# Performance work log

Measured on AMD Instinct MI355X. Metric: run time of the kernel, lower is better.

## Reference

```python
import jax, jax.numpy as jnp
import numpy as np

B, S, D, H, L, F = 1, 2048, 768, 12, 2, 3072
DH = D // H          # 64
W = 256              # one-sided sliding window (attention_window=512 total)
NC = S // W          # number of query chunks
VOCAB = 50265


def _ln(x, s, b, eps=1e-5):
    m = x.mean(-1, keepdims=True)
    v = ((x - m) ** 2).mean(-1, keepdims=True)
    return (x - m) / jnp.sqrt(v + eps) * s + b


def setup_inputs() -> dict:
    key = jax.random.key(0)
    ks = jax.random.split(key, 16)
    p = lambda k, sh: jax.random.normal(k, sh, jnp.float32) * 0.02
    return {
        "input_ids": jax.random.randint(ks[0], (B, S), 0, VOCAB),
        "attention_mask": jnp.ones((B, S), jnp.int32),
        "word_emb": p(ks[1], (VOCAB, D)),
        "pos_emb": p(ks[2], (S + 2, D)),          # roberta-style pos ids start at 2
        "type_emb": p(ks[3], (1, D)),
        "emb_ln_s": jnp.ones((D,), jnp.float32),
        "emb_ln_b": jnp.zeros((D,), jnp.float32),
        "Wqkv": p(ks[4], (L, 3, D, D)),
        "bqkv": jnp.zeros((L, 3, D), jnp.float32),
        "Wo": p(ks[5], (L, D, D)),
        "bo": jnp.zeros((L, D), jnp.float32),
        "ln1_s": jnp.ones((L, D), jnp.float32),
        "ln1_b": jnp.zeros((L, D), jnp.float32),
        "W1": p(ks[6], (L, D, F)),
        "b1": jnp.zeros((L, F), jnp.float32),
        "W2": p(ks[7], (L, F, D)),
        "b2": jnp.zeros((L, D), jnp.float32),
        "ln2_s": jnp.ones((L, D), jnp.float32),
        "ln2_b": jnp.zeros((L, D), jnp.float32),
        "pool_W": p(ks[8], (D, D)),
        "pool_b": jnp.zeros((D,), jnp.float32),
    }


def reference(input_ids, attention_mask, word_emb, pos_emb, type_emb,
              emb_ln_s, emb_ln_b, Wqkv, bqkv, Wo, bo, ln1_s, ln1_b,
              W1, b1, W2, b2, ln2_s, ln2_b, pool_W, pool_b):
    # ---- embeddings (roberta/longformer style) ----
    pos_ids = jnp.cumsum(attention_mask, axis=1) * attention_mask + 1  # padding_idx=1
    x = word_emb[input_ids] + pos_emb[pos_ids] + type_emb[0]
    x = _ln(x, emb_ln_s, emb_ln_b)

    # ---- banded-attention index/mask precompute (int constants) ----
    idx = jnp.arange(NC)[:, None] * W + jnp.arange(3 * W)[None, :]      # [NC, 3W] into padded seq
    rel = (jnp.arange(3 * W)[None, :] - W) - jnp.arange(W)[:, None]     # key_pos - query_pos
    band = (rel >= -W) & (rel <= W)                                      # [W, 3W]
    kmask = jnp.pad(attention_mask, ((0, 0), (W, W)))[:, idx].astype(bool)  # [B, NC, 3W]
    valid = band[None, None] & kmask[:, :, None, :]                      # [B, NC, W, 3W]

    inv_sqrt_dh = 1.0 / np.sqrt(DH)
    for l in range(L):
        qkv = jnp.einsum('bsd,tde->tbse', x, Wqkv[l]) + bqkv[l][:, None, None, :]
        q, k, v = [t.reshape(B, S, H, DH).transpose(0, 2, 1, 3) for t in qkv]  # [B,H,S,DH]
        qc = q.reshape(B, H, NC, W, DH)
        kp = jnp.pad(k, ((0, 0), (0, 0), (W, W), (0, 0)))
        vp = jnp.pad(v, ((0, 0), (0, 0), (W, W), (0, 0)))
        kc = kp[:, :, idx]                                               # [B,H,NC,3W,DH]
        vc = vp[:, :, idx]
        scores = jnp.einsum('bhcqd,bhckd->bhcqk', qc, kc) * inv_sqrt_dh  # [B,H,NC,W,3W]
        scores = jnp.where(valid[:, None], scores, -1e9)
        attn = jax.nn.softmax(scores, axis=-1)
        ctx = jnp.einsum('bhcqk,bhckd->bhcqd', attn, vc)
        ctx = ctx.reshape(B, H, S, DH).transpose(0, 2, 1, 3).reshape(B, S, D)
        x = _ln(x + ctx @ Wo[l] + bo[l], ln1_s[l], ln1_b[l])
        h = jax.nn.gelu(x @ W1[l] + b1[l], approximate=False)
        x = _ln(x + h @ W2[l] + b2[l], ln2_s[l], ln2_b[l])

    pooled = jnp.tanh(x[:, 0] @ pool_W + pool_b)
    return x, pooled
```

## Files before the change

### kernel.cpp

```cpp
#include <hip/hip_runtime.h>
#include <hip/hip_bf16.h>
#include <math.h>
#include <stddef.h>
#include <stdint.h>

typedef __hip_bfloat16 bf16;
typedef short bf16x8 __attribute__((ext_vector_type(8)));
typedef float f32x4 __attribute__((ext_vector_type(4)));

#define CS 2048
#define CD 768
#define CH 12
#define CDH 64
#define CF 3072
#define CW 256
#define CL 2
#define QKVN 2304
#define SDC ((size_t)CS * CD)
#define EPS_LD 136

__device__ __forceinline__ void gload_lds16(const bf16* g, bf16* l) {
  __builtin_amdgcn_global_load_lds(
      (const __attribute__((address_space(1))) void*)g,
      (__attribute__((address_space(3))) void*)l, 16, 0, 0);
}

__device__ __forceinline__ unsigned short f2bu(float v) {
  bf16 b = __float2bfloat16(v);
  return *(unsigned short*)&b;
}
__device__ __forceinline__ float bu2f(unsigned short u) {
  bf16 b = *(bf16*)&u;
  return __bfloat162float(b);
}

template<int NW>
__device__ __forceinline__ float block_reduce_sum(float v, float* buf) {
  #pragma unroll
  for (int off = 32; off > 0; off >>= 1) v += __shfl_down(v, off, 64);
  __syncthreads();
  if ((threadIdx.x & 63) == 0) buf[threadIdx.x >> 6] = v;
  __syncthreads();
  float s = buf[0];
  #pragma unroll
  for (int w = 1; w < NW; ++w) s += buf[w];
  return s;
}

__global__ __launch_bounds__(256) void prep_kernel(
    const float* __restrict__ Wqkv, const float* __restrict__ Wo,
    const float* __restrict__ W1, const float* __restrict__ W2,
    bf16* __restrict__ WqkvT, bf16* __restrict__ WoT,
    bf16* __restrict__ W1T, bf16* __restrict__ W2T,
    const int* __restrict__ ids, const int* __restrict__ mask,
    const float* __restrict__ wemb, const float* __restrict__ pemb,
    const float* __restrict__ temb, const float* __restrict__ gs,
    const float* __restrict__ gb, float* __restrict__ x, bf16* __restrict__ xb) {
  __shared__ float tile[64][33];
  __shared__ float red[4];
  int b = blockIdx.x;
  if (b < 6912) {
    const float* src; bf16* dst; int K, N, t;
    if (b < 1728) {
      int mat = b / 288; t = b % 288; K = 768; N = 768;
      src = Wqkv + (size_t)mat * 768 * 768; dst = WqkvT + (size_t)mat * 768 * 768;
    } else if (b < 2304) {
      b -= 1728; int mat = b / 288; t = b % 288; K = 768; N = 768;
      src = Wo + (size_t)mat * 768 * 768; dst = WoT + (size_t)mat * 768 * 768;
    } else if (b < 4608) {
      b -= 2304; int mat = b / 1152; t = b % 1152; K = 768; N = 3072;
      src = W1 + (size_t)mat * 768 * 3072; dst = W1T + (size_t)mat * 768 * 3072;
    } else {
      b -= 4608; int mat = b / 1152; t = b % 1152; K = 3072; N = 768;
      src = W2 + (size_t)mat * 3072 * 768; dst = W2T + (size_t)mat * 3072 * 768;
    }
    int nt = N / 32;
    int bn = (t % nt) * 32, bk = (t / nt) * 64;
    int tx = threadIdx.x & 31, ty = (threadIdx.x >> 5);
    #pragma unroll
    for (int i = 0; i < 8; ++i)
      tile[ty + i * 8][tx] = src[(size_t)(bk + ty + i * 8) * N + bn + tx];
    __syncthreads();
    #pragma unroll
    for (int i = 0; i < 4; ++i) {
      int n = ty + i * 8;
      if (n < 32) {
        ushort2 pk;
        pk.x = f2bu(tile[2 * tx][n]);
        pk.y = f2bu(tile[2 * tx + 1][n]);
        *(ushort2*)&dst[(size_t)(bn + n) * K + bk + 2 * tx] = pk;
      }
    }
  } else {
    int srow = b - 6912;
    int t = threadIdx.x;
    float ps = 0.f;
    for (int i = t; i <= srow; i += 256) ps += (float)mask[i];
    float tot = block_reduce_sum<4>(ps, red);
    long long pid = (long long)((int)(tot + 0.5f) * mask[srow] + 1);
    long long id = ids[srow];
    float4 v = {0.f, 0.f, 0.f, 0.f};
    if (t < 192) {
      int d = t * 4;
      float4 a = *(const float4*)&wemb[id * CD + d];
      float4 p = *(const float4*)&pemb[pid * CD + d];
      float4 tm = *(const float4*)&temb[d];
      v.x = a.x + p.x + tm.x; v.y = a.y + p.y + tm.y;
      v.z = a.z + p.z + tm.z; v.w = a.w + p.w + tm.w;
    }
    float sum = block_reduce_sum<4>(v.x + v.y + v.z + v.w, red);
    float mean = sum * (1.0f / CD);
    float cx = v.x - mean, cy = v.y - mean, cz = v.z - mean, cw = v.w - mean;
    float sqv = (t < 192) ? (cx * cx + cy * cy + cz * cz + cw * cw) : 0.f;
    float sq = block_reduce_sum<4>(sqv, red);
    float rstd = rsqrtf(sq * (1.0f / CD) + 1e-5f);
    if (t < 192) {
      int d = t * 4;
      float4 g4 = *(const float4*)&gs[d];
      float4 b4 = *(const float4*)&gb[d];
      float4 o;
      o.x = cx * rstd * g4.x + b4.x;
      o.y = cy * rstd * g4.y + b4.y;
      o.z = cz * rstd * g4.z + b4.z;
      o.w = cw * rstd * g4.w + b4.w;
      *(float4*)&x[(size_t)srow * CD + d] = o;
      ushort4 pk;
      pk.x = f2bu(o.x); pk.y = f2bu(o.y); pk.z = f2bu(o.z); pk.w = f2bu(o.w);
      *(ushort4*)&xb[(size_t)srow * CD + d] = pk;
    }
  }
}

template<int GELU, int SPLITS, int TRANS>
__device__ __forceinline__ void gemm_body(
    const bf16* __restrict__ A, const bf16* __restrict__ Bt,
    const float* __restrict__ bias, bf16* __restrict__ Cout,
    bf16* __restrict__ vTout, int M, int N, int Ktot, char* smem,
    int bx, int by) {
  bf16* As = (bf16*)smem;
  bf16* Bs = (bf16*)(smem + 16384);
  bf16* eps = (bf16*)smem;
  const int tid = threadIdx.x;
  const int wave = tid >> 6, lane = tid & 63;
  const int m0 = by * 64, n0 = bx * 128;
  const int wn = wave * 64;
  const int quad = lane >> 4, rsel = lane & 15;
  const int rx = rsel & 7;
  const int r_in = lane >> 3;
  const int chunk = lane & 7;
  const int gchunk = chunk ^ r_in;
  const int Klen = Ktot / SPLITS;
  const int koff = (SPLITS > 1) ? blockIdx.z * Klen : 0;
  const int nt = Klen / 64;

  f32x4 acc[4][4] = {};

  auto STAGE = [&](int buf, int t) {
    const int kk = koff + t * 64;
    bf16* Asb = As + buf * 4096;
    bf16* Bsb = Bs + buf * 8192;
    #pragma unroll
    for (int i = 0; i < 12; ++i) {
      int op = wave * 12 + i;
      if (op < 8) {
        int row = op * 8 + r_in;
        gload_lds16(A + (size_t)(m0 + row) * Ktot + kk + gchunk * 8, &Asb[op * 512]);
      } else {
        int row = (op - 8) * 8 + r_in;
        gload_lds16(Bt + (size_t)(n0 + row) * Ktot + kk + gchunk * 8, &Bsb[(op - 8) * 512]);
      }
    }
  };

  STAGE(0, 0);
  __asm__ volatile("s_waitcnt vmcnt(0)" ::: "memory");
  __builtin_amdgcn_s_barrier();
  __builtin_amdgcn_sched_barrier(0);

  int cur = 0;
  for (int t = 0; t < nt; ++t) {
    if (t + 1 < nt) STAGE(cur ^ 1, t + 1);
    __builtin_amdgcn_sched_barrier(0);
    const bf16* Asb = As + cur * 4096;
    const bf16* Bsb = Bs + cur * 8192;
    #pragma unroll
    for (int kh = 0; kh < 2; ++kh) {
      bf16x8 af[4], bfr[4];
      int cq = ((kh << 2) | quad);
      #pragma unroll
      for (int i = 0; i < 4; ++i)
        af[i] = *(const bf16x8*)&Asb[(i * 16 + rsel) * 64 + (cq ^ rx) * 8];
      #pragma unroll
      for (int j = 0; j < 4; ++j)
        bfr[j] = *(const bf16x8*)&Bsb[(wn + j * 16 + rsel) * 64 + (cq ^ rx) * 8];
      #pragma unroll
      for (int i = 0; i < 4; ++i)
        #pragma unroll
        for (int j = 0; j < 4; ++j) {
          if (TRANS)
            acc[i][j] = __builtin_amdgcn_mfma_f32_16x16x32_bf16(af[i], bfr[j], acc[i][j], 0, 0, 0);
          else
            acc[i][j] = __builtin_amdgcn_mfma_f32_16x16x32_bf16(bfr[j], af[i], acc[i][j], 0, 0, 0);
        }
    }
    __asm__ volatile("s_waitcnt vmcnt(0)" ::: "memory");
    __builtin_amdgcn_s_barrier();
    __builtin_amdgcn_sched_barrier(0);
    cur ^= 1;
  }

  if (!TRANS) {
    #pragma unroll
    for (int j = 0; j < 4; ++j) {
      int cb = wn + j * 16 + quad * 4;
      float4 bv = {0.f, 0.f, 0.f, 0.f};
      if (SPLITS == 1 || blockIdx.z == 0) bv = *(const float4*)&bias[n0 + cb];
      #pragma unroll
      for (int i = 0; i < 4; ++i) {
        float v0 = acc[i][j][0] + bv.x;
        float v1 = acc[i][j][1] + bv.y;
        float v2 = acc[i][j][2] + bv.z;
        float v3 = acc[i][j][3] + bv.w;
        if (GELU) {
          v0 = 0.5f * v0 * (1.0f + erff(v0 * 0.70710678118654752f));
          v1 = 0.5f * v1 * (1.0f + erff(v1 * 0.70710678118654752f));
          v2 = 0.5f * v2 * (1.0f + erff(v2 * 0.70710678118654752f));
          v3 = 0.5f * v3 * (1.0f + erff(v3 * 0.70710678118654752f));
        }
        ushort4 pk;
        pk.x = f2bu(v0); pk.y = f2bu(v1); pk.z = f2bu(v2); pk.w = f2bu(v3);
        *(ushort4*)&eps[(i * 16 + rsel) * EPS_LD + cb] = pk;
      }
    }
    __syncthreads();
    const size_t zb = (SPLITS > 1) ? (size_t)blockIdx.z * M * N : 0;
    #pragma unroll
    for (int it = 0; it < 8; ++it) {
      int row = it * 8 + (tid >> 4);
      int c = tid & 15;
      bf16x8 v = *(const bf16x8*)&eps[row * EPS_LD + c * 8];
      *(bf16x8*)&Cout[zb + (size_t)(m0 + row) * N + n0 + c * 8] = v;
    }
  } else {
    #pragma unroll
    for (int j = 0; j < 4; ++j) {
      float bv = bias[n0 + wn + j * 16 + rsel];
      #pragma unroll
      for (int i = 0; i < 4; ++i) {
        ushort4 pk;
        pk.x = f2bu(acc[i][j][0] + bv);
        pk.y = f2bu(acc[i][j][1] + bv);
        pk.z = f2bu(acc[i][j][2] + bv);
        pk.w = f2bu(acc[i][j][3] + bv);
        *(ushort4*)&eps[(wn + j * 16 + rsel) * 72 + i * 16 + quad * 4] = pk;
      }
    }
    __syncthreads();
    #pragma unroll
    for (int it = 0; it < 8; ++it) {
      int row = it * 16 + (tid >> 3);
      int c = tid & 7;
      bf16x8 v = *(const bf16x8*)&eps[row * 72 + c * 8];
      *(bf16x8*)&vTout[(size_t)(n0 - 1536 + row) * CS + m0 + c * 8] = v;
    }
  }
}

template<int GELU, int SPLITS, int VTFUSE>
__global__ __launch_bounds__(128, 3) void gemm_mfma(
    const bf16* __restrict__ A, const bf16* __restrict__ Bt,
    const float* __restrict__ bias, bf16* __restrict__ Cout,
    bf16* __restrict__ vTout, int M, int N, int Ktot) {
  __shared__ __align__(16) char smem[49152];
  int nx = gridDim.x, ny = gridDim.y;
  int nwg = nx * ny;
  int orig = blockIdx.x + blockIdx.y * nx;
  int bx, by;
  if (nwg & 7) { bx = blockIdx.x; by = blockIdx.y; }
  else {
    int q8 = nwg >> 3;
    int nid = (orig & 7) * q8 + (orig >> 3);
    bx = nid / ny; by = nid - bx * ny;
  }
  if (VTFUSE && bx * 128 >= 1536)
    gemm_body<0, 1, 1>(A, Bt, bias, Cout, vTout, M, N, Ktot, smem, bx, by);
  else
    gemm_body<GELU, SPLITS, 0>(A, Bt, bias, Cout, vTout, M, N, Ktot, smem, bx, by);
}

__global__ __launch_bounds__(256) void attn_mfma(
    const bf16* __restrict__ qkv, const bf16* __restrict__ vT,
    const int* __restrict__ mask, bf16* __restrict__ ctx) {
  __shared__ __align__(16) bf16 Ks[64 * 64];
  __shared__ __align__(16) bf16 Vs[64 * 64];
  __shared__ __align__(16) bf16 Ps[4][16][72];
  const int h = blockIdx.y;
  const int q0 = blockIdx.x * 64;
  const int tid = threadIdx.x;
  const int wv = tid >> 6, lane = tid & 63;
  const int quad = lane >> 4, rsel = lane & 15;
  const int rx = rsel & 7;
  const int qw = q0 + wv * 16;
  const int r_in = lane >> 3, chunk = lane & 7, gchunk = chunk ^ r_in;

  const bf16* qp = &qkv[(size_t)(qw + rsel) * QKVN + h * CDH + quad * 8];
  bf16x8 qf0 = *(const bf16x8*)qp;
  bf16x8 qf1 = *(const bf16x8*)(qp + 32);

  float mi[4], li[4];
  f32x4 o[4] = {};
  #pragma unroll
  for (int r = 0; r < 4; ++r) { mi[r] = -1e30f; li[r] = 0.f; }

  #pragma unroll 1
  for (int kt = 0; kt < 9; ++kt) {
    int kbase = q0 - CW + kt * 64;
    bool tile_in = (kbase + 63 >= 0) && (kbase < CS);
    if (tile_in) {
      #pragma unroll
      for (int i = 0; i < 4; ++i) {
        int op = wv * 4 + i;
        if (op < 8) {
          int krow = min(max(kbase + op * 8 + r_in, 0), CS - 1);
          gload_lds16(&qkv[(size_t)krow * QKVN + 768 + h * CDH + gchunk * 8], &Ks[op * 512]);
        } else {
          int vop = op - 8;
          int kc = min(max(kbase + gchunk * 8, 0), CS - 8);
          gload_lds16(&vT[(size_t)(h * CDH + vop * 8 + r_in) * CS + kc], &Vs[vop * 512]);
        }
      }
    }
    __syncthreads();
    bool active = tile_in && (kbase + 63 >= qw - CW) && (kbase <= qw + 15 + CW);
    if (active) {
      f32x4 sc[4];
      #pragma unroll
      for (int nt = 0; nt < 4; ++nt) {
        const bf16* kp = &Ks[(nt * 16 + rsel) * 64];
        bf16x8 kf0 = *(const bf16x8*)(kp + (quad ^ rx) * 8);
        bf16x8 kf1 = *(const bf16x8*)(kp + ((quad + 4) ^ rx) * 8);
        f32x4 z = {};
        __builtin_amdgcn_s_setprio(1);
        z = __builtin_amdgcn_mfma_f32_16x16x32_bf16(qf0, kf0, z, 0, 0, 0);
        z = __builtin_amdgcn_mfma_f32_16x16x32_bf16(qf1, kf1, z, 0, 0, 0);
        __builtin_amdgcn_s_setprio(0);
        sc[nt] = z;
      }
      float mx[4] = {-1e30f, -1e30f, -1e30f, -1e30f};
      #pragma unroll
      for (int nt = 0; nt < 4; ++nt) {
        int pp = kbase + nt * 16 + rsel;
        int ppc = min(max(pp, 0), CS - 1);
        bool kvld = (pp >= 0) && (pp < CS) && (mask[ppc] != 0);
        #pragma unroll
        for (int r = 0; r < 4; ++r) {
          int qr = qw + quad * 4 + r;
          float s = sc[nt][r] * 0.125f;
          bool band = (pp >= qr - CW) && (pp <= qr + CW);
          s = (kvld && band) ? s : -1e9f;
          sc[nt][r] = s;
          mx[r] = fmaxf(mx[r], s);
        }
      }
      #pragma unroll
      for (int r = 0; r < 4; ++r) {
        #pragma unroll
        for (int off = 1; off < 16; off <<= 1)
          mx[r] = fmaxf(mx[r], __shfl_xor(mx[r], off, 64));
      }
      float al[4], rs[4] = {};
      #pragma unroll
      for (int r = 0; r < 4; ++r) {
        float mn = fmaxf(mi[r], mx[r]);
        al[r] = __expf(mi[r] - mn);
        mi[r] = mn;
      }
      #pragma unroll
      for (int nt = 0; nt < 4; ++nt)
        #pragma unroll
        for (int r = 0; r < 4; ++r) {
          float p = __expf(sc[nt][r] - mi[r]);
          sc[nt][r] = p;
          rs[r] += p;
        }
      #pragma unroll
      for (int r = 0; r < 4; ++r) {
        #pragma unroll
        for (int off = 1; off < 16; off <<= 1)
          rs[r] += __shfl_xor(rs[r], off, 64);
        li[r] = li[r] * al[r] + rs[r];
      }
      #pragma unroll
      for (int d = 0; d < 4; ++d)
        #pragma unroll
        for (int r = 0; r < 4; ++r) o[d][r] *= al[r];
      #pragma unroll
      for (int nt = 0; nt < 4; ++nt)
        #pragma unroll
        for (int r = 0; r < 4; ++r)
          Ps[wv][quad * 4 + r][nt * 16 + rsel] = __float2bfloat16(sc[nt][r]);
      __asm__ volatile("s_waitcnt lgkmcnt(0)" ::: "memory");
      __builtin_amdgcn_sched_barrier(0);
      bf16x8 pf0 = *(const bf16x8*)&Ps[wv][rsel][quad * 8];
      bf16x8 pf1 = *(const bf16x8*)&Ps[wv][rsel][32 + quad * 8];
      #pragma unroll
      for (int d = 0; d < 4; ++d) {
        const bf16* vr = &Vs[(d * 16 + rsel) * 64];
        bf16x8 vf0 = *(const bf16x8*)(vr + (quad ^ rx) * 8);
        bf16x8 vf1 = *(const bf16x8*)(vr + ((quad + 4) ^ rx) * 8);
        __builtin_amdgcn_s_setprio(1);
        o[d] = __builtin_amdgcn_mfma_f32_16x16x32_bf16(pf0, vf0, o[d], 0, 0, 0);
        o[d] = __builtin_amdgcn_mfma_f32_16x16x32_bf16(pf1, vf1, o[d], 0, 0, 0);
        __builtin_amdgcn_s_setprio(0);
      }
    }
    __syncthreads();
  }

  float inv[4];
  #pragma unroll
  for (int r = 0; r < 4; ++r) inv[r] = 1.0f / li[r];
  #pragma unroll
  for (int d = 0; d < 4; ++d)
    #pragma unroll
    for (int r = 0; r < 4; ++r)
      Ps[wv][quad * 4 + r][d * 16 + rsel] = __float2bfloat16(o[d][r] * inv[r]);
  __asm__ volatile("s_waitcnt lgkmcnt(0)" ::: "memory");
  __builtin_amdgcn_sched_barrier(0);
  #pragma unroll
  for (int it = 0; it < 2; ++it) {
    int row = it * 8 + (lane >> 3);
    bf16x8 vv = *(const bf16x8*)&Ps[wv][row][(lane & 7) * 8];
    *(bf16x8*)&ctx[(size_t)(qw + row) * CD + h * CDH + (lane & 7) * 8] = vv;
  }
}

template<int P>
__global__ __launch_bounds__(192) void add_ln_kernel(
    const bf16* __restrict__ g, const float* __restrict__ xin,
    float* __restrict__ xout, bf16* __restrict__ xb,
    const float* __restrict__ gs, const float* __restrict__ gb) {
  __shared__ float red[3];
  int srow = blockIdx.x;
  int d = threadIdx.x * 4;
  size_t base = (size_t)srow * CD + d;
  float4 a = *(const float4*)&xin[base];
  #pragma unroll
  for (int p = 0; p < P; ++p) {
    ushort4 gg = *(const ushort4*)&g[p * SDC + base];
    a.x += bu2f(gg.x); a.y += bu2f(gg.y); a.z += bu2f(gg.z); a.w += bu2f(gg.w);
  }
  float sum = block_reduce_sum<3>(a.x + a.y + a.z + a.w, red);
  float mean = sum * (1.0f / CD);
  float cx = a.x - mean, cy = a.y - mean, cz = a.z - mean, cw = a.w - mean;
  float sq = block_reduce_sum<3>(cx * cx + cy * cy + cz * cz + cw * cw, red);
  float rstd = rsqrtf(sq * (1.0f / CD) + 1e-5f);
  float4 g4 = *(const float4*)&gs[d];
  float4 b4 = *(const float4*)&gb[d];
  float4 o;
  o.x = cx * rstd * g4.x + b4.x;
  o.y = cy * rstd * g4.y + b4.y;
  o.z = cz * rstd * g4.z + b4.z;
  o.w = cw * rstd * g4.w + b4.w;
  *(float4*)&xout[base] = o;
  ushort4 pk;
  pk.x = f2bu(o.x); pk.y = f2bu(o.y); pk.z = f2bu(o.z); pk.w = f2bu(o.w);
  *(ushort4*)&xb[base] = pk;
}

__global__ __launch_bounds__(256) void pool_kernel(
    const float* __restrict__ x, const float* __restrict__ Wp,
    const float* __restrict__ bp, float* __restrict__ out) {
  __shared__ float xs[CD];
  __shared__ float red[4][64];
  int t = threadIdx.x;
  for (int i = t; i < CD; i += 256) xs[i] = x[i];
  __syncthreads();
  int n = blockIdx.x * 64 + (t & 63);
  int kp = t >> 6;
  float acc = 0.f;
  #pragma unroll 4
  for (int kk = kp * 192; kk < kp * 192 + 192; ++kk)
    acc = fmaf(xs[kk], Wp[(size_t)kk * CD + n], acc);
  red[kp][t & 63] = acc;
  __syncthreads();
  if (t < 64) {
    int nn = blockIdx.x * 64 + t;
    out[nn] = tanhf(red[0][t] + red[1][t] + red[2][t] + red[3][t] + bp[nn]);
  }
}

extern "C" void kernel_launch(void* const* d_in, const int* in_sizes, int n_in,
                              void* d_out, int out_size, void* d_ws, size_t ws_size,
                              hipStream_t stream) {
  const int*   ids   = (const int*)d_in[0];
  const int*   mask  = (const int*)d_in[1];
  const float* wemb  = (const float*)d_in[2];
  const float* pemb  = (const float*)d_in[3];
  const float* temb  = (const float*)d_in[4];
  const float* elns  = (const float*)d_in[5];
  const float* elnb  = (const float*)d_in[6];
  const float* Wqkv  = (const float*)d_in[7];
  const float* bqkv  = (const float*)d_in[8];
  const float* Wo    = (const float*)d_in[9];
  const float* bo    = (const float*)d_in[10];
  const float* ln1s  = (const float*)d_in[11];
  const float* ln1b  = (const float*)d_in[12];
  const float* W1    = (const float*)d_in[13];
  const float* b1    = (const float*)d_in[14];
  const float* W2    = (const float*)d_in[15];
  const float* b2    = (const float*)d_in[16];
  const float* ln2s  = (const float*)d_in[17];
  const float* ln2b  = (const float*)d_in[18];
  const float* poolW = (const float*)d_in[19];
  const float* poolb = (const float*)d_in[20];

  const size_t SD = SDC;
  const size_t SF = (size_t)CS * CF;

  char* w = (char*)d_ws;
  float* x    = (float*)w; w += SD * 4;
  bf16*  xb   = (bf16*)w;  w += SD * 2;
  bf16*  qkv  = (bf16*)w;  w += (size_t)CS * QKVN * 2;
  bf16*  vT   = (bf16*)w;  w += SD * 2;
  bf16*  ctxb = (bf16*)w;  w += SD * 2;
  bf16*  t1b  = (bf16*)w;  w += SF * 2;
  bf16*  t2   = (bf16*)w;  w += SD * 2 * 4;
  bf16* WqkvT = (bf16*)w;  w += (size_t)CL * QKVN * CD * 2;
  bf16* WoT   = (bf16*)w;  w += (size_t)CL * CD * CD * 2;
  bf16* W1T   = (bf16*)w;  w += (size_t)CL * CF * CD * 2;
  bf16* W2T   = (bf16*)w;  w += (size_t)CL * CD * CF * 2;

  prep_kernel<<<6912 + CS, 256, 0, stream>>>(
      Wqkv, Wo, W1, W2, WqkvT, WoT, W1T, W2T,
      ids, mask, wemb, pemb, temb, elns, elnb, x, xb);

  for (int l = 0; l < CL; ++l) {
    gemm_mfma<0,1,1><<<dim3(QKVN/128, CS/64), 128, 0, stream>>>(
        xb, WqkvT + (size_t)l * QKVN * CD, bqkv + (size_t)l * 3 * CD, qkv, vT, CS, QKVN, CD);
    attn_mfma<<<dim3(CS/64, CH), 256, 0, stream>>>(qkv, vT, mask, ctxb);
    gemm_mfma<0,2,0><<<dim3(CD/128, CS/64, 2), 128, 0, stream>>>(
        ctxb, WoT + (size_t)l * CD * CD, bo + (size_t)l * CD, t2, nullptr, CS, CD, CD);
    add_ln_kernel<2><<<CS, 192, 0, stream>>>(t2, x, x, xb,
        ln1s + (size_t)l * CD, ln1b + (size_t)l * CD);
    gemm_mfma<1,1,0><<<dim3(CF/128, CS/64), 128, 0, stream>>>(
        xb, W1T + (size_t)l * CF * CD, b1 + (size_t)l * CF, t1b, nullptr, CS, CF, CD);
    gemm_mfma<0,2,0><<<dim3(CD/128, CS/64, 2), 128, 0, stream>>>(
        t1b, W2T + (size_t)l * CD * CF, b2 + (size_t)l * CD, t2, nullptr, CS, CD, CF);
    float* lastx = (l == CL - 1) ? (float*)d_out : x;
    add_ln_kernel<2><<<CS, 192, 0, stream>>>(t2, x, lastx, xb,
        ln2s + (size_t)l * CD, ln2b + (size_t)l * CD);
  }

  pool_kernel<<<12, 256, 0, stream>>>((float*)d_out, poolW, poolb, (float*)d_out + SD);
}
```

Measured before the change: 512.6 us.

## Use 128x128 block tiles with four waves for QKV and FFN1 GEMMs

Templates the GEMM body on the M tile size and adds a 128-row variant that uses 4 waves in a 2x2 arrangement of 64x64 warp tiles, with shared memory and epilogue indexing generalised to match. The QKV projection and first FFN GEMM switch to this variant to raise operand reuse per loaded byte and cut global traffic. The trade-off is larger LDS use per block, lower occupancy, and fewer blocks in the grid, which may underfill the CUs.

Measured after the change: 508.2 us. No clear change (-0.8%).

```diff
diff --git a/kernel.cpp b/kernel.cpp
--- a/kernel.cpp
+++ b/kernel.cpp
@@ -131,19 +131,24 @@
   }
 }
 
-template<int GELU, int SPLITS, int TRANS>
+template<int BM, int GELU, int SPLITS, int TRANS>
 __device__ __forceinline__ void gemm_body(
     const bf16* __restrict__ A, const bf16* __restrict__ Bt,
     const float* __restrict__ bias, bf16* __restrict__ Cout,
     bf16* __restrict__ vTout, int M, int N, int Ktot, char* smem,
     int bx, int by) {
+  constexpr int NW = BM / 32;
+  constexpr int A_OPS = BM / 8;
+  constexpr int OPW = (A_OPS + 16) / NW;
+  constexpr int AS_STRIDE = BM * 64;
   bf16* As = (bf16*)smem;
-  bf16* Bs = (bf16*)(smem + 16384);
+  bf16* Bs = (bf16*)(smem + AS_STRIDE * 2 * 2);
   bf16* eps = (bf16*)smem;
   const int tid = threadIdx.x;
   const int wave = tid >> 6, lane = tid & 63;
-  const int m0 = by * 64, n0 = bx * 128;
-  const int wn = wave * 64;
+  const int m0 = by * BM, n0 = bx * 128;
+  const int wm = (BM == 64) ? 0 : (wave & 1) * 64;
+  const int wn = (BM == 64) ? wave * 64 : (wave >> 1) * 64;
   const int quad = lane >> 4, rsel = lane & 15;
   const int rx = rsel & 7;
   const int r_in = lane >> 3;
@@ -157,17 +162,17 @@
 
   auto STAGE = [&](int buf, int t) {
     const int kk = koff + t * 64;
-    bf16* Asb = As + buf * 4096;
+    bf16* Asb = As + buf * AS_STRIDE;
     bf16* Bsb = Bs + buf * 8192;
     #pragma unroll
-    for (int i = 0; i < 12; ++i) {
-      int op = wave * 12 + i;
-      if (op < 8) {
+    for (int i = 0; i < OPW; ++i) {
+      int op = wave * OPW + i;
+      if (op < A_OPS) {
         int row = op * 8 + r_in;
         gload_lds16(A + (size_t)(m0 + row) * Ktot + kk + gchunk * 8, &Asb[op * 512]);
       } else {
-        int row = (op - 8) * 8 + r_in;
-        gload_lds16(Bt + (size_t)(n0 + row) * Ktot + kk + gchunk * 8, &Bsb[(op - 8) * 512]);
+        int row = (op - A_OPS) * 8 + r_in;
+        gload_lds16(Bt + (size_t)(n0 + row) * Ktot + kk + gchunk * 8, &Bsb[(op - A_OPS) * 512]);
       }
     }
   };
@@ -181,7 +186,7 @@
   for (int t = 0; t < nt; ++t) {
     if (t + 1 < nt) STAGE(cur ^ 1, t + 1);
     __builtin_amdgcn_sched_barrier(0);
-    const bf16* Asb = As + cur * 4096;
+    const bf16* Asb = As + cur * AS_STRIDE;
     const bf16* Bsb = Bs + cur * 8192;
     #pragma unroll
     for (int kh = 0; kh < 2; ++kh) {
@@ -189,7 +194,7 @@
       int cq = ((kh << 2) | quad);
       #pragma unroll
       for (int i = 0; i < 4; ++i)
-        af[i] = *(const bf16x8*)&Asb[(i * 16 + rsel) * 64 + (cq ^ rx) * 8];
+        af[i] = *(const bf16x8*)&Asb[(wm + i * 16 + rsel) * 64 + (cq ^ rx) * 8];
       #pragma unroll
       for (int j = 0; j < 4; ++j)
         bfr[j] = *(const bf16x8*)&Bsb[(wn + j * 16 + rsel) * 64 + (cq ^ rx) * 8];
@@ -229,14 +234,14 @@
         }
         ushort4 pk;
         pk.x = f2bu(v0); pk.y = f2bu(v1); pk.z = f2bu(v2); pk.w = f2bu(v3);
-        *(ushort4*)&eps[(i * 16 + rsel) * EPS_LD + cb] = pk;
+        *(ushort4*)&eps[(wm + i * 16 + rsel) * EPS_LD + cb] = pk;
       }
     }
     __syncthreads();
     const size_t zb = (SPLITS > 1) ? (size_t)blockIdx.z * M * N : 0;
     #pragma unroll
     for (int it = 0; it < 8; ++it) {
-      int row = it * 8 + (tid >> 4);
+      int row = it * (BM / 8) + (tid >> 4);
       int c = tid & 15;
       bf16x8 v = *(const bf16x8*)&eps[row * EPS_LD + c * 8];
       *(bf16x8*)&Cout[zb + (size_t)(m0 + row) * N + n0 + c * 8] = v;
@@ -252,26 +257,27 @@
         pk.y = f2bu(acc[i][j][1] + bv);
         pk.z = f2bu(acc[i][j][2] + bv);
         pk.w = f2bu(acc[i][j][3] + bv);
-        *(ushort4*)&eps[(wn + j * 16 + rsel) * 72 + i * 16 + quad * 4] = pk;
+        *(ushort4*)&eps[(wn + j * 16 + rsel) * EPS_LD + wm + i * 16 + quad * 4] = pk;
       }
     }
     __syncthreads();
     #pragma unroll
     for (int it = 0; it < 8; ++it) {
-      int row = it * 16 + (tid >> 3);
-      int c = tid & 7;
-      bf16x8 v = *(const bf16x8*)&eps[row * 72 + c * 8];
+      int row, c;
+      if (BM == 64) { row = it * 16 + (tid >> 3); c = tid & 7; }
+      else          { row = it * 16 + (tid >> 4); c = tid & 15; }
+      bf16x8 v = *(const bf16x8*)&eps[row * EPS_LD + c * 8];
       *(bf16x8*)&vTout[(size_t)(n0 - 1536 + row) * CS + m0 + c * 8] = v;
     }
   }
 }
 
-template<int GELU, int SPLITS, int VTFUSE>
-__global__ __launch_bounds__(128, 3) void gemm_mfma(
+template<int BM, int GELU, int SPLITS, int VTFUSE>
+__global__ __launch_bounds__(BM * 2, BM == 64 ? 3 : 2) void gemm_mfma(
     const bf16* __restrict__ A, const bf16* __restrict__ Bt,
     const float* __restrict__ bias, bf16* __restrict__ Cout,
     bf16* __restrict__ vTout, int M, int N, int Ktot) {
-  __shared__ __align__(16) char smem[49152];
+  __shared__ __align__(16) char smem[BM * 256 + 32768];
   int nx = gridDim.x, ny = gridDim.y;
   int nwg = nx * ny;
   int orig = blockIdx.x + blockIdx.y * nx;
@@ -283,9 +289,9 @@
     bx = nid / ny; by = nid - bx * ny;
   }
   if (VTFUSE && bx * 128 >= 1536)
-    gemm_body<0, 1, 1>(A, Bt, bias, Cout, vTout, M, N, Ktot, smem, bx, by);
+    gemm_body<BM, 0, 1, 1>(A, Bt, bias, Cout, vTout, M, N, Ktot, smem, bx, by);
   else
-    gemm_body<GELU, SPLITS, 0>(A, Bt, bias, Cout, vTout, M, N, Ktot, smem, bx, by);
+    gemm_body<BM, GELU, SPLITS, 0>(A, Bt, bias, Cout, vTout, M, N, Ktot, smem, bx, by);
 }
 
 __global__ __launch_bounds__(256) void attn_mfma(
@@ -536,16 +542,16 @@
       ids, mask, wemb, pemb, temb, elns, elnb, x, xb);
 
   for (int l = 0; l < CL; ++l) {
-    gemm_mfma<0,1,1><<<dim3(QKVN/128, CS/64), 128, 0, stream>>>(
+    gemm_mfma<128,0,1,1><<<dim3(QKVN/128, CS/128), 256, 0, stream>>>(
         xb, WqkvT + (size_t)l * QKVN * CD, bqkv + (size_t)l * 3 * CD, qkv, vT, CS, QKVN, CD);
     attn_mfma<<<dim3(CS/64, CH), 256, 0, stream>>>(qkv, vT, mask, ctxb);
-    gemm_mfma<0,2,0><<<dim3(CD/128, CS/64, 2), 128, 0, stream>>>(
+    gemm_mfma<64,0,2,0><<<dim3(CD/128, CS/64, 2), 128, 0, stream>>>(
         ctxb, WoT + (size_t)l * CD * CD, bo + (size_t)l * CD, t2, nullptr, CS, CD, CD);
     add_ln_kernel<2><<<CS, 192, 0, stream>>>(t2, x, x, xb,
         ln1s + (size_t)l * CD, ln1b + (size_t)l * CD);
-    gemm_mfma<1,1,0><<<dim3(CF/128, CS/64), 128, 0, stream>>>(
+    gemm_mfma<128,1,1,0><<<dim3(CF/128, CS/128), 256, 0, stream>>>(
         xb, W1T + (size_t)l * CF * CD, b1 + (size_t)l * CF, t1b, nullptr, CS, CF, CD);
-    gemm_mfma<0,2,0><<<dim3(CD/128, CS/64, 2), 128, 0, stream>>>(
+    gemm_mfma<64,0,2,0><<<dim3(CD/128, CS/64, 2), 128, 0, stream>>>(
         t1b, W2T + (size_t)l * CD * CF, b2 + (size_t)l * CD, t2, nullptr, CS, CD, CF);
     float* lastx = (l == CL - 1) ? (float*)d_out : x;
     add_ln_kernel<2><<<CS, 192, 0, stream>>>(t2, x, lastx, xb,
```
